# Kernel tuning notes

Hardware: AMD Instinct MI355X
Metric: run time of the kernel (lower is better)

Reference implementation:

```python
import jax, jax.numpy as jnp
import numpy as np

H, I, E, TOP_K = 2048, 1408, 16, 6
IS = 2816  # shared-expert intermediate = moe_intermediate_size * n_shared_experts
NORM_TOPK_PROB = False


def _silu_and_mul(gate_up):
    # gate_up: [..., 2*I] -> silu(gate) * up, [..., I]
    d = gate_up.shape[-1] // 2
    g, u = gate_up[..., :d], gate_up[..., d:]
    return jax.nn.silu(g) * u


def setup_inputs() -> dict:
    key = jax.random.key(0)
    ks = jax.random.split(key, 6)
    s = 0.02
    return {
        "x": jax.random.normal(ks[0], (1, 2048, H), jnp.float32),
        "gate_w": jax.random.normal(ks[1], (E, H), jnp.float32) * s,
        "w1": jax.random.normal(ks[2], (E, 2 * I, H), jnp.float32) * s,
        "w2": jax.random.normal(ks[3], (E, H, I), jnp.float32) * s,
        "shared_w1": jax.random.normal(ks[4], (2 * IS, H), jnp.float32) * s,
        "shared_w2": jax.random.normal(ks[5], (H, IS), jnp.float32) * s,
    }


def reference(x, gate_w, w1, w2, shared_w1, shared_w2):
    B, S, Hd = x.shape
    xf = x.reshape(-1, Hd)  # [T, H]
    T = xf.shape[0]

    # shared experts (dense MLP over all tokens)
    shared_out = _silu_and_mul(xf @ shared_w1.T) @ shared_w2.T  # [T, H]

    # router: softmax in fp32, then top-k
    logits = xf @ gate_w.T  # [T, E]
    probs = jax.nn.softmax(logits.astype(jnp.float32), axis=-1)
    routing_weights, selected = jax.lax.top_k(probs, TOP_K)  # [T, k]
    if NORM_TOPK_PROB:
        routing_weights = routing_weights / routing_weights.sum(-1, keepdims=True)

    # scatter top-k weights into dense [T, E] combine matrix (fused_moe equivalent)
    combine = jnp.zeros((T, E), jnp.float32).at[
        jnp.arange(T)[:, None], selected
    ].add(routing_weights).astype(x.dtype)

    # expert MLPs, combined with routing weights
    gate_up = jnp.einsum('th,eoh->teo', xf, w1)  # [T, E, 2I]
    act = _silu_and_mul(gate_up)                 # [T, E, I]
    moe_out = jnp.einsum('te,tei,ehi->th', combine, act, w2)  # [T, H]

    return (moe_out + shared_out).reshape(B, S, Hd)
```

## Files before the change

### kernel.cpp

```cpp
#include <hip/hip_runtime.h>
#include <hip/hip_bf16.h>
#include <cstdint>
#include <cstddef>


typedef __bf16 bf16;
typedef __bf16 bf16x8 __attribute__((ext_vector_type(8)));
typedef float  f32x4  __attribute__((ext_vector_type(4)));

constexpr int Hdim  = 2048;
constexpr int Idim  = 1408;
constexpr int NE    = 16;
constexpr int TOPK  = 6;
constexpr int ISdim = 2816;
constexpr int Ttok  = 2048;
constexpr int BMT   = 256;
constexpr int MAX_SLOTS = 16384;

__device__ __forceinline__ void gll16(const void* g, void* l) {
  __builtin_amdgcn_global_load_lds((__attribute__((address_space(1))) void*)(g),
                                   (__attribute__((address_space(3))) void*)(l),
                                   16, 0, 0);
}


__global__ void init_kernel(int* cnt, int* fill, int* tok_of_slot, float* wt_of_slot) {
  int i = blockIdx.x * 256 + threadIdx.x;
  if (i < NE) { cnt[i] = 0; fill[i] = 0; }
  if (i < MAX_SLOTS) { tok_of_slot[i] = -1; wt_of_slot[i] = 0.f; }
}

__global__ void cvt_kernel(const float* __restrict__ src, bf16* __restrict__ dst, int n8) {
  int i = blockIdx.x * 256 + threadIdx.x;
  if (i >= n8) return;
  f32x4 f0 = *(const f32x4*)(src + (size_t)i * 8);
  f32x4 f1 = *(const f32x4*)(src + (size_t)i * 8 + 4);
  bf16x8 v;
#pragma unroll
  for (int j = 0; j < 4; j++) { v[j] = (bf16)f0[j]; v[j + 4] = (bf16)f1[j]; }
  *(bf16x8*)(dst + (size_t)i * 8) = v;
}

__global__ void router_kernel(const float* __restrict__ x, const float* __restrict__ gw,
                              int* __restrict__ sel_e, float* __restrict__ sel_w,
                              int* __restrict__ cnt) {
  int t = blockIdx.x;
  int lane = threadIdx.x;
  const float* xr = x + (size_t)t * Hdim;
  float acc[NE];
#pragma unroll
  for (int e = 0; e < NE; e++) acc[e] = 0.f;
  for (int h = lane; h < Hdim; h += 64) {
    float xv = xr[h];
#pragma unroll
    for (int e = 0; e < NE; e++) acc[e] += xv * gw[e * Hdim + h];
  }
#pragma unroll
  for (int e = 0; e < NE; e++) {
#pragma unroll
    for (int off = 32; off > 0; off >>= 1) acc[e] += __shfl_xor(acc[e], off, 64);
  }
  if (lane == 0) {
    float m = acc[0];
#pragma unroll
    for (int e = 1; e < NE; e++) m = fmaxf(m, acc[e]);
    float p[NE]; float s = 0.f;
#pragma unroll
    for (int e = 0; e < NE; e++) { p[e] = __expf(acc[e] - m); s += p[e]; }
    float inv = 1.f / s;
    bool used[NE];
#pragma unroll
    for (int e = 0; e < NE; e++) used[e] = false;
    for (int k = 0; k < TOPK; k++) {
      int best = 0; float bv = -1.f;
      for (int e = 0; e < NE; e++) if (!used[e] && p[e] > bv) { bv = p[e]; best = e; }
      used[best] = true;
      sel_e[t * TOPK + k] = best;
      sel_w[t * TOPK + k] = bv * inv;
      atomicAdd(&cnt[best], 1);
    }
  }
}

__global__ void scan_kernel(const int* __restrict__ cnt, int* __restrict__ pbase,
                            int* __restrict__ mtiles) {
  if (threadIdx.x == 0 && blockIdx.x == 0) {
    int pb = 0;
    for (int e = 0; e < NE; e++) {
      pbase[e] = pb;
      int mt = (cnt[e] + BMT - 1) / BMT;
      mtiles[e] = mt;
      pb += mt * BMT;
    }
  }
}

__global__ void assign_kernel(const int* __restrict__ sel_e, const float* __restrict__ sel_w,
                              const int* __restrict__ pbase, int* __restrict__ fill,
                              int* __restrict__ tok_of_slot, float* __restrict__ wt_of_slot,
                              int* __restrict__ slot_of) {
  int i = blockIdx.x * 256 + threadIdx.x;
  if (i >= Ttok * TOPK) return;
  int e = sel_e[i];
  int t = i / TOPK;
  int pos = atomicAdd(&fill[e], 1);
  int slot = pbase[e] + pos;
  tok_of_slot[slot] = t;
  wt_of_slot[slot] = sel_w[i];
  slot_of[i] = slot;
}


template <int BM>
__global__ __launch_bounds__(256, 2)
void gateup_kernel(const bf16* __restrict__ Abase,
                   const bf16* __restrict__ w1b, const bf16* __restrict__ sw1b,
                   bf16* __restrict__ actx, bf16* __restrict__ acts,
                   const int* __restrict__ tok_of_slot, const float* __restrict__ wt_of_slot,
                   const int* __restrict__ pbase, const int* __restrict__ mtiles) {
  constexpr int NQ = BM / 64;
  constexpr int WROWS = BM / 4;
  constexpr int NI = WROWS / 16;
  constexpr int K = Hdim;
  const int z = blockIdx.z;
  const bool SH = (z == NE);
  const bf16* Wb; bf16* C; int Isz, row0;
  if (SH) {
    Wb = sw1b; C = acts; Isz = ISdim;
    row0 = blockIdx.y * BM;
  } else {
    if (blockIdx.x >= Idim / 64) return;
    if ((int)blockIdx.y >= mtiles[z]) return;
    Wb = w1b + (size_t)z * 2 * Idim * Hdim; C = actx; Isz = Idim;
    row0 = pbase[z] + blockIdx.y * BM;
  }
  const int col0 = blockIdx.x * 64;
  const int tid = threadIdx.x;
  const int lane = tid & 63;
  const int wv = tid >> 6;
  const int m16 = lane & 15, quad = lane >> 4;

  __shared__ __align__(16) bf16 ldsA[2][BM * 32];
  __shared__ __align__(16) bf16 ldsG[2][64 * 32];
  __shared__ __align__(16) bf16 ldsU[2][64 * 32];

  const int srow = tid >> 2;
  const int scol = (tid & 3) * 8;

  const bf16* aptr[NQ];
#pragma unroll
  for (int q = 0; q < NQ; q++) {
    int r = row0 + q * 64 + srow;
    int tok = SH ? r : tok_of_slot[r];
    if (tok < 0) tok = 0;
    aptr[q] = Abase + (size_t)tok * K + scol;
  }
  const bf16* gptr = Wb + (size_t)(col0 + srow) * K + scol;
  const bf16* uptr = Wb + (size_t)(Isz + col0 + srow) * K + scol;

  f32x4 accg[NI][4], accu[NI][4];
#pragma unroll
  for (int i = 0; i < NI; i++)
#pragma unroll
    for (int j = 0; j < 4; j++)
#pragma unroll
      for (int r = 0; r < 4; r++) { accg[i][j][r] = 0.f; accu[i][j][r] = 0.f; }

  auto stage = [&](int b, int k) {
    gll16(gptr + k, &ldsG[b][tid * 8]);
    gll16(uptr + k, &ldsU[b][tid * 8]);
#pragma unroll
    for (int q = 0; q < NQ; q++) gll16(aptr[q] + k, &ldsA[b][q * 2048 + tid * 8]);
  };

  stage(0, 0);
  __syncthreads();
  for (int k0 = 0; k0 < K; k0 += 32) {
    const int cur = (k0 >> 5) & 1;
    if (k0 + 32 < K) stage(cur ^ 1, k0 + 32);
    bf16x8 af[NI], gf[4], uf[4];
#pragma unroll
    for (int i = 0; i < NI; i++)
      af[i] = *(const bf16x8*)(&ldsA[cur][(wv * WROWS + i * 16 + m16) * 32 + quad * 8]);
#pragma unroll
    for (int j = 0; j < 4; j++) {
      gf[j] = *(const bf16x8*)(&ldsG[cur][(j * 16 + m16) * 32 + quad * 8]);
      uf[j] = *(const bf16x8*)(&ldsU[cur][(j * 16 + m16) * 32 + quad * 8]);
    }
#pragma unroll
    for (int i = 0; i < NI; i++)
#pragma unroll
      for (int j = 0; j < 4; j++) {
        accg[i][j] = __builtin_amdgcn_mfma_f32_16x16x32_bf16(af[i], gf[j], accg[i][j], 0, 0, 0);
        accu[i][j] = __builtin_amdgcn_mfma_f32_16x16x32_bf16(af[i], uf[j], accu[i][j], 0, 0, 0);
      }
    __syncthreads();
  }

#pragma unroll
  for (int i = 0; i < NI; i++) {
#pragma unroll
    for (int r = 0; r < 4; r++) {
      int grow = row0 + wv * WROWS + i * 16 + quad * 4 + r;
      float scale = SH ? 1.f : wt_of_slot[grow];
#pragma unroll
      for (int j = 0; j < 4; j++) {
        float g = accg[i][j][r];
        float u = accu[i][j][r];
        float a = g * u * scale / (1.f + __expf(-g));
        C[(size_t)grow * Isz + (col0 + j * 16 + m16)] = (bf16)a;
      }
    }
  }
}


template <int BM>
__global__ __launch_bounds__(256, 2)
void down_kernel(const bf16* __restrict__ actx, const bf16* __restrict__ acts,
                 const bf16* __restrict__ w2b, const bf16* __restrict__ sw2b,
                 float* __restrict__ slot_out, float* __restrict__ out,
                 const int* __restrict__ pbase, const int* __restrict__ mtiles) {
  constexpr int NQ = BM / 64;
  constexpr int WROWS = BM / 4;
  constexpr int NI = WROWS / 16;
  const int z = blockIdx.z;
  const bool SH = (z == NE);
  const bf16* A; const bf16* Wb; float* dst; int K, row0;
  if (SH) {
    A = acts; Wb = sw2b; dst = out; K = ISdim;
    row0 = blockIdx.y * BM;
  } else {
    if ((int)blockIdx.y >= mtiles[z]) return;
    A = actx; Wb = w2b + (size_t)z * Hdim * Idim; dst = slot_out; K = Idim;
    row0 = pbase[z] + blockIdx.y * BM;
  }
  const int col0 = blockIdx.x * 128;
  const int tid = threadIdx.x;
  const int lane = tid & 63;
  const int wv = tid >> 6;
  const int m16 = lane & 15, quad = lane >> 4;

  __shared__ __align__(16) bf16 ldsA[2][BM * 32];
  __shared__ __align__(16) bf16 ldsB[2][128 * 32];

  const int srow = tid >> 2;
  const int scol = (tid & 3) * 8;

  const bf16* aptr[NQ];
#pragma unroll
  for (int q = 0; q < NQ; q++)
    aptr[q] = A + (size_t)(row0 + q * 64 + srow) * K + scol;
  const bf16* bptr[2];
#pragma unroll
  for (int q = 0; q < 2; q++)
    bptr[q] = Wb + (size_t)(col0 + q * 64 + srow) * K + scol;

  f32x4 acc[NI][8];
#pragma unroll
  for (int i = 0; i < NI; i++)
#pragma unroll
    for (int j = 0; j < 8; j++)
#pragma unroll
      for (int r = 0; r < 4; r++) acc[i][j][r] = 0.f;

  auto stage = [&](int b, int k) {
#pragma unroll
    for (int q = 0; q < 2; q++) gll16(bptr[q] + k, &ldsB[b][q * 2048 + tid * 8]);
#pragma unroll
    for (int q = 0; q < NQ; q++) gll16(aptr[q] + k, &ldsA[b][q * 2048 + tid * 8]);
  };

  stage(0, 0);
  __syncthreads();
  for (int k0 = 0; k0 < K; k0 += 32) {
    const int cur = (k0 >> 5) & 1;
    if (k0 + 32 < K) stage(cur ^ 1, k0 + 32);
    bf16x8 af[NI], bfr[8];
#pragma unroll
    for (int i = 0; i < NI; i++)
      af[i] = *(const bf16x8*)(&ldsA[cur][(wv * WROWS + i * 16 + m16) * 32 + quad * 8]);
#pragma unroll
    for (int j = 0; j < 8; j++)
      bfr[j] = *(const bf16x8*)(&ldsB[cur][(j * 16 + m16) * 32 + quad * 8]);
#pragma unroll
    for (int i = 0; i < NI; i++)
#pragma unroll
      for (int j = 0; j < 8; j++)
        acc[i][j] = __builtin_amdgcn_mfma_f32_16x16x32_bf16(af[i], bfr[j], acc[i][j], 0, 0, 0);
    __syncthreads();
  }

#pragma unroll
  for (int i = 0; i < NI; i++) {
#pragma unroll
    for (int r = 0; r < 4; r++) {
      int grow = row0 + wv * WROWS + i * 16 + quad * 4 + r;
      float* orow = dst + (size_t)grow * Hdim;
#pragma unroll
      for (int j = 0; j < 8; j++) orow[col0 + j * 16 + m16] = acc[i][j][r];
    }
  }
}


__global__ void combine_kernel(const float* __restrict__ slot_out,
                               const int* __restrict__ slot_of,
                               float* __restrict__ out) {
  const int t = blockIdx.x;
  const int c = threadIdx.x * 8;
  float* op = out + (size_t)t * Hdim + c;
  f32x4 a0 = *(const f32x4*)op;
  f32x4 a1 = *(const f32x4*)(op + 4);
#pragma unroll
  for (int k = 0; k < TOPK; k++) {
    int s = slot_of[t * TOPK + k];
    const float* sp = slot_out + (size_t)s * Hdim + c;
    f32x4 b0 = *(const f32x4*)sp;
    f32x4 b1 = *(const f32x4*)(sp + 4);
    a0 += b0; a1 += b1;
  }
  *(f32x4*)op = a0;
  *(f32x4*)(op + 4) = a1;
}


extern "C" void kernel_launch(void* const* d_in, const int* in_sizes, int n_in,
                              void* d_out, int out_size, void* d_ws, size_t ws_size,
                              hipStream_t stream) {
  (void)in_sizes; (void)n_in; (void)out_size; (void)ws_size;
  const float* x   = (const float*)d_in[0];
  const float* gw  = (const float*)d_in[1];
  const float* w1  = (const float*)d_in[2];
  const float* w2  = (const float*)d_in[3];
  const float* sw1 = (const float*)d_in[4];
  const float* sw2 = (const float*)d_in[5];
  float* out = (float*)d_out;

  char* ws = (char*)d_ws;
  size_t off = 0;
  auto alloc = [&](size_t bytes) -> void* {
    void* p = ws + off;
    off += (bytes + 255) & ~(size_t)255;
    return p;
  };
  int*   cnt   = (int*)alloc(NE * 4);
  int*   fill  = (int*)alloc(NE * 4);
  int*   pbase = (int*)alloc(NE * 4);
  int*   mtl   = (int*)alloc(NE * 4);
  int*   sel_e = (int*)alloc((size_t)Ttok * TOPK * 4);
  float* sel_w = (float*)alloc((size_t)Ttok * TOPK * 4);
  int*   slotf = (int*)alloc((size_t)Ttok * TOPK * 4);
  int*   tok   = (int*)alloc((size_t)MAX_SLOTS * 4);
  float* wt    = (float*)alloc((size_t)MAX_SLOTS * 4);
  bf16*  xb    = (bf16*)alloc((size_t)Ttok * Hdim * 2);
  bf16*  actx  = (bf16*)alloc((size_t)MAX_SLOTS * Idim * 2);
  bf16*  acts  = (bf16*)alloc((size_t)Ttok * ISdim * 2);

  const size_t n_w1  = (size_t)NE * 2 * Idim * Hdim;
  const size_t n_w2  = (size_t)NE * Hdim * Idim;
  const size_t n_sw1 = (size_t)2 * ISdim * Hdim;
  const size_t n_sw2 = (size_t)Hdim * ISdim;
  bf16* w1b  = (bf16*)alloc(n_w1 * 2);
  bf16* w2b  = (bf16*)alloc(n_w2 * 2);
  bf16* sw1b = (bf16*)alloc(n_sw1 * 2);
  bf16* sw2b = (bf16*)alloc(n_sw2 * 2);
  float* slot_out = (float*)w1b;

  init_kernel<<<(MAX_SLOTS + 255) / 256, 256, 0, stream>>>(cnt, fill, tok, wt);
  cvt_kernel<<<((int)(Ttok * (size_t)Hdim / 8) + 255) / 256, 256, 0, stream>>>(x, xb, Ttok * Hdim / 8);
  router_kernel<<<Ttok, 64, 0, stream>>>(x, gw, sel_e, sel_w, cnt);
  scan_kernel<<<1, 64, 0, stream>>>(cnt, pbase, mtl);
  assign_kernel<<<(Ttok * TOPK + 255) / 256, 256, 0, stream>>>(sel_e, sel_w, pbase, fill, tok, wt, slotf);

  cvt_kernel<<<((int)(n_w1 / 8) + 255) / 256, 256, 0, stream>>>(w1, w1b, (int)(n_w1 / 8));
  cvt_kernel<<<((int)(n_w2 / 8) + 255) / 256, 256, 0, stream>>>(w2, w2b, (int)(n_w2 / 8));
  cvt_kernel<<<((int)(n_sw1 / 8) + 255) / 256, 256, 0, stream>>>(sw1, sw1b, (int)(n_sw1 / 8));
  cvt_kernel<<<((int)(n_sw2 / 8) + 255) / 256, 256, 0, stream>>>(sw2, sw2b, (int)(n_sw2 / 8));

  gateup_kernel<BMT><<<dim3(ISdim / 64, Ttok / BMT, NE + 1), 256, 0, stream>>>(
      xb, w1b, sw1b, actx, acts, tok, wt, pbase, mtl);
  down_kernel<BMT><<<dim3(Hdim / 128, Ttok / BMT, NE + 1), 256, 0, stream>>>(
      actx, acts, w2b, sw2b, slot_out, out, pbase, mtl);
  combine_kernel<<<Ttok, Hdim / 8, 0, stream>>>(slot_out, slotf, out);
}
```

Measured before the change: 1.468 ms.

## Triple-buffer GEMM K-loop with vmcnt waits, swizzle LDS, flatten XCD-aware grid

```diff
diff --git a/kernel.cpp b/kernel.cpp
--- a/kernel.cpp
+++ b/kernel.cpp
@@ -17,11 +17,21 @@
 constexpr int BMT   = 256;
 constexpr int MAX_SLOTS = 16384;
 
+constexpr int GU_R    = 2816;
+constexpr int GU_GRID = 3168;
+constexpr int GU_CHNK = GU_GRID / 8;
+constexpr int DN_R    = 2048;
+constexpr int DN_GRID = 2176;
+constexpr int DN_CHNK = DN_GRID / 8;
+
 __device__ __forceinline__ void gll16(const void* g, void* l) {
   __builtin_amdgcn_global_load_lds((__attribute__((address_space(1))) void*)(g),
                                    (__attribute__((address_space(3))) void*)(l),
                                    16, 0, 0);
 }
+
+#define WAITVM(N) do { asm volatile("s_waitcnt vmcnt(" #N ")" ::: "memory"); \
+                       __builtin_amdgcn_sched_barrier(0); } while (0)
 
 
 __global__ void init_kernel(int* cnt, int* fill, int* tok_of_slot, float* wt_of_slot) {
@@ -111,41 +121,48 @@
 }
 
 
-template <int BM>
 __global__ __launch_bounds__(256, 2)
 void gateup_kernel(const bf16* __restrict__ Abase,
                    const bf16* __restrict__ w1b, const bf16* __restrict__ sw1b,
                    bf16* __restrict__ actx, bf16* __restrict__ acts,
                    const int* __restrict__ tok_of_slot, const float* __restrict__ wt_of_slot,
                    const int* __restrict__ pbase, const int* __restrict__ mtiles) {
+  constexpr int BM = BMT;
   constexpr int NQ = BM / 64;
   constexpr int WROWS = BM / 4;
   constexpr int NI = WROWS / 16;
   constexpr int K = Hdim;
-  const int z = blockIdx.z;
-  const bool SH = (z == NE);
+  constexpr int NT = K / 32;
+
+  const int l = ((int)blockIdx.x & 7) * GU_CHNK + ((int)blockIdx.x >> 3);
+  bool SH; int e = 0, xt, mt;
+  if (l < GU_R) {
+    SH = false;
+    e = l / 176; int r = l - e * 176;
+    xt = r >> 3; mt = r & 7;
+    if (mt >= mtiles[e]) return;
+  } else {
+    SH = true;
+    int ls = l - GU_R;
+    xt = ls >> 3; mt = ls & 7;
+  }
   const bf16* Wb; bf16* C; int Isz, row0;
-  if (SH) {
-    Wb = sw1b; C = acts; Isz = ISdim;
-    row0 = blockIdx.y * BM;
-  } else {
-    if (blockIdx.x >= Idim / 64) return;
-    if ((int)blockIdx.y >= mtiles[z]) return;
-    Wb = w1b + (size_t)z * 2 * Idim * Hdim; C = actx; Isz = Idim;
-    row0 = pbase[z] + blockIdx.y * BM;
-  }
-  const int col0 = blockIdx.x * 64;
+  if (SH) { Wb = sw1b; C = acts; Isz = ISdim; row0 = mt * BM; }
+  else    { Wb = w1b + (size_t)e * 2 * Idim * Hdim; C = actx; Isz = Idim;
+            row0 = pbase[e] + mt * BM; }
+  const int col0 = xt * 64;
+
   const int tid = threadIdx.x;
   const int lane = tid & 63;
   const int wv = tid >> 6;
   const int m16 = lane & 15, quad = lane >> 4;
 
-  __shared__ __align__(16) bf16 ldsA[2][BM * 32];
-  __shared__ __align__(16) bf16 ldsG[2][64 * 32];
-  __shared__ __align__(16) bf16 ldsU[2][64 * 32];
+  __shared__ __align__(16) bf16 ldsA[3][BM * 32];
+  __shared__ __align__(16) bf16 ldsG[3][64 * 32];
+  __shared__ __align__(16) bf16 ldsU[3][64 * 32];
 
   const int srow = tid >> 2;
-  const int scol = (tid & 3) * 8;
+  const int scol = ((tid & 3) ^ ((srow >> 1) & 3)) * 8;
 
   const bf16* aptr[NQ];
 #pragma unroll
@@ -173,19 +190,31 @@
     for (int q = 0; q < NQ; q++) gll16(aptr[q] + k, &ldsA[b][q * 2048 + tid * 8]);
   };
 
+  const int qsw8 = (quad ^ ((m16 >> 1) & 3)) * 8;
+
   stage(0, 0);
-  __syncthreads();
-  for (int k0 = 0; k0 < K; k0 += 32) {
-    const int cur = (k0 >> 5) & 1;
-    if (k0 + 32 < K) stage(cur ^ 1, k0 + 32);
+  stage(1, 32);
+#pragma unroll 1
+  for (int ks = 0; ks < NT; ks++) {
+    const int cur = ks % 3;
+    if (ks + 2 < NT) {
+      int nb = cur + 2; if (nb >= 3) nb -= 3;
+      stage(nb, (ks + 2) * 32);
+      WAITVM(12);
+    } else if (ks + 2 == NT) {
+      WAITVM(6);
+    } else {
+      WAITVM(0);
+    }
+    __builtin_amdgcn_s_barrier();
     bf16x8 af[NI], gf[4], uf[4];
 #pragma unroll
     for (int i = 0; i < NI; i++)
-      af[i] = *(const bf16x8*)(&ldsA[cur][(wv * WROWS + i * 16 + m16) * 32 + quad * 8]);
+      af[i] = *(const bf16x8*)(&ldsA[cur][(wv * WROWS + i * 16 + m16) * 32 + qsw8]);
 #pragma unroll
     for (int j = 0; j < 4; j++) {
-      gf[j] = *(const bf16x8*)(&ldsG[cur][(j * 16 + m16) * 32 + quad * 8]);
-      uf[j] = *(const bf16x8*)(&ldsU[cur][(j * 16 + m16) * 32 + quad * 8]);
+      gf[j] = *(const bf16x8*)(&ldsG[cur][(j * 16 + m16) * 32 + qsw8]);
+      uf[j] = *(const bf16x8*)(&ldsU[cur][(j * 16 + m16) * 32 + qsw8]);
     }
 #pragma unroll
     for (int i = 0; i < NI; i++)
@@ -194,7 +223,7 @@
         accg[i][j] = __builtin_amdgcn_mfma_f32_16x16x32_bf16(af[i], gf[j], accg[i][j], 0, 0, 0);
         accu[i][j] = __builtin_amdgcn_mfma_f32_16x16x32_bf16(af[i], uf[j], accu[i][j], 0, 0, 0);
       }
-    __syncthreads();
+    __builtin_amdgcn_s_barrier();
   }
 
 #pragma unroll
@@ -215,37 +244,45 @@
 }
 
 
-template <int BM>
 __global__ __launch_bounds__(256, 2)
 void down_kernel(const bf16* __restrict__ actx, const bf16* __restrict__ acts,
                  const bf16* __restrict__ w2b, const bf16* __restrict__ sw2b,
                  float* __restrict__ slot_out, float* __restrict__ out,
                  const int* __restrict__ pbase, const int* __restrict__ mtiles) {
+  constexpr int BM = BMT;
   constexpr int NQ = BM / 64;
   constexpr int WROWS = BM / 4;
   constexpr int NI = WROWS / 16;
-  const int z = blockIdx.z;
-  const bool SH = (z == NE);
+
+  const int l = ((int)blockIdx.x & 7) * DN_CHNK + ((int)blockIdx.x >> 3);
+  bool SH; int e = 0, xt, mt;
+  if (l < DN_R) {
+    SH = false;
+    e = l >> 7; int r = l & 127;
+    xt = r >> 3; mt = r & 7;
+    if (mt >= mtiles[e]) return;
+  } else {
+    SH = true;
+    int ls = l - DN_R;
+    xt = ls >> 3; mt = ls & 7;
+  }
   const bf16* A; const bf16* Wb; float* dst; int K, row0;
-  if (SH) {
-    A = acts; Wb = sw2b; dst = out; K = ISdim;
-    row0 = blockIdx.y * BM;
-  } else {
-    if ((int)blockIdx.y >= mtiles[z]) return;
-    A = actx; Wb = w2b + (size_t)z * Hdim * Idim; dst = slot_out; K = Idim;
-    row0 = pbase[z] + blockIdx.y * BM;
-  }
-  const int col0 = blockIdx.x * 128;
+  if (SH) { A = acts; Wb = sw2b; dst = out; K = ISdim; row0 = mt * BM; }
+  else    { A = actx; Wb = w2b + (size_t)e * Hdim * Idim; dst = slot_out; K = Idim;
+            row0 = pbase[e] + mt * BM; }
+  const int NT = K / 32;
+  const int col0 = xt * 128;
+
   const int tid = threadIdx.x;
   const int lane = tid & 63;
   const int wv = tid >> 6;
   const int m16 = lane & 15, quad = lane >> 4;
 
-  __shared__ __align__(16) bf16 ldsA[2][BM * 32];
-  __shared__ __align__(16) bf16 ldsB[2][128 * 32];
+  __shared__ __align__(16) bf16 ldsA[3][BM * 32];
+  __shared__ __align__(16) bf16 ldsB[3][128 * 32];
 
   const int srow = tid >> 2;
-  const int scol = (tid & 3) * 8;
+  const int scol = ((tid & 3) ^ ((srow >> 1) & 3)) * 8;
 
   const bf16* aptr[NQ];
 #pragma unroll
@@ -271,24 +308,36 @@
     for (int q = 0; q < NQ; q++) gll16(aptr[q] + k, &ldsA[b][q * 2048 + tid * 8]);
   };
 
+  const int qsw8 = (quad ^ ((m16 >> 1) & 3)) * 8;
+
   stage(0, 0);
-  __syncthreads();
-  for (int k0 = 0; k0 < K; k0 += 32) {
-    const int cur = (k0 >> 5) & 1;
-    if (k0 + 32 < K) stage(cur ^ 1, k0 + 32);
+  stage(1, 32);
+#pragma unroll 1
+  for (int ks = 0; ks < NT; ks++) {
+    const int cur = ks % 3;
+    if (ks + 2 < NT) {
+      int nb = cur + 2; if (nb >= 3) nb -= 3;
+      stage(nb, (ks + 2) * 32);
+      WAITVM(12);
+    } else if (ks + 2 == NT) {
+      WAITVM(6);
+    } else {
+      WAITVM(0);
+    }
+    __builtin_amdgcn_s_barrier();
     bf16x8 af[NI], bfr[8];
 #pragma unroll
     for (int i = 0; i < NI; i++)
-      af[i] = *(const bf16x8*)(&ldsA[cur][(wv * WROWS + i * 16 + m16) * 32 + quad * 8]);
+      af[i] = *(const bf16x8*)(&ldsA[cur][(wv * WROWS + i * 16 + m16) * 32 + qsw8]);
 #pragma unroll
     for (int j = 0; j < 8; j++)
-      bfr[j] = *(const bf16x8*)(&ldsB[cur][(j * 16 + m16) * 32 + quad * 8]);
+      bfr[j] = *(const bf16x8*)(&ldsB[cur][(j * 16 + m16) * 32 + qsw8]);
 #pragma unroll
     for (int i = 0; i < NI; i++)
 #pragma unroll
       for (int j = 0; j < 8; j++)
         acc[i][j] = __builtin_amdgcn_mfma_f32_16x16x32_bf16(af[i], bfr[j], acc[i][j], 0, 0, 0);
-    __syncthreads();
+    __builtin_amdgcn_s_barrier();
   }
 
 #pragma unroll
@@ -378,9 +427,7 @@
   cvt_kernel<<<((int)(n_sw1 / 8) + 255) / 256, 256, 0, stream>>>(sw1, sw1b, (int)(n_sw1 / 8));
   cvt_kernel<<<((int)(n_sw2 / 8) + 255) / 256, 256, 0, stream>>>(sw2, sw2b, (int)(n_sw2 / 8));
 
-  gateup_kernel<BMT><<<dim3(ISdim / 64, Ttok / BMT, NE + 1), 256, 0, stream>>>(
-      xb, w1b, sw1b, actx, acts, tok, wt, pbase, mtl);
-  down_kernel<BMT><<<dim3(Hdim / 128, Ttok / BMT, NE + 1), 256, 0, stream>>>(
-      actx, acts, w2b, sw2b, slot_out, out, pbase, mtl);
+  gateup_kernel<<<GU_GRID, 256, 0, stream>>>(xb, w1b, sw1b, actx, acts, tok, wt, pbase, mtl);
+  down_kernel<<<DN_GRID, 256, 0, stream>>>(actx, acts, w2b, sw2b, slot_out, out, pbase, mtl);
   combine_kernel<<<Ttok, Hdim / 8, 0, stream>>>(slot_out, slotf, out);
 }
```

Measured after the change: 1.616 ms. +10.1%, slower.
